# Optimization experiments

Measured on AMD Instinct MI355X. Metric: run time of the kernel, lower is better.

The kernel has to match this reference:

```python
import jax, jax.numpy as jnp
import numpy as np

N_NODES = 50000
N_EDGES = 800000
D = 128
N_LAYERS = 3
N_GRAPHS = 256


def setup_inputs() -> dict:
    key = jax.random.key(0)
    ks = jax.random.split(key, 6)
    x = jax.random.normal(ks[0], (N_NODES, D), dtype=jnp.float32)
    edge_index = jax.random.randint(ks[1], (2, N_EDGES), 0, N_NODES, dtype=jnp.int64)
    batch = jnp.sort(jax.random.randint(ks[2], (N_NODES,), 0, N_GRAPHS, dtype=jnp.int64))
    # Xavier-uniform linear weights (bias filled with 0 per weights_init)
    limit = float(np.sqrt(6.0 / (D + D)))
    W1 = jax.random.uniform(ks[3], (N_LAYERS, D, D), jnp.float32, -limit, limit)
    W2 = jax.random.uniform(ks[4], (N_LAYERS, D, D), jnp.float32, -limit, limit)
    b1 = jnp.zeros((N_LAYERS, D), jnp.float32)
    b2 = jnp.zeros((N_LAYERS, D), jnp.float32)
    return {"x": x, "edge_index": edge_index, "batch": batch,
            "W1": W1, "b1": b1, "W2": W2, "b2": b2}


def reference(x, edge_index, batch, W1, b1, W2, b2):
    src, dst = edge_index[0], edge_index[1]
    h = x  # [N, D]
    pools = []
    for i in range(N_LAYERS):
        # GINConv, eps=0: (1+eps)*h + sum of neighbor (source) features at target
        agg = jax.ops.segment_sum(h[src], dst, num_segments=N_NODES)  # [N, D]
        h = h + agg
        # MLP: Linear -> ReLU -> Linear, then outer ReLU activation
        h = jnp.maximum(h @ W1[i] + b1[i], 0.0) @ W2[i] + b2[i]
        h = jnp.maximum(h, 0.0)
        # global_add_pool over graph ids
        pools.append(jax.ops.segment_sum(h, batch, num_segments=N_GRAPHS))
    return jnp.concatenate(pools, axis=1)  # [N_GRAPHS, N_LAYERS*D]
```

## Files before the change

### kernel.cpp

```cpp
#include <hip/hip_runtime.h>

#define N_NODES 50000
#define N_EDGES 800000
#define DIM 128
#define N_LAYERS 3
#define N_GRAPHS 256
#define OUT_COLS (N_LAYERS * DIM)

#define SUBS 4
#define SUBCAP 24
#define ROWSTRIDE (SUBS * SUBCAP)

#define FILL_NB 3125
#define X2H_NB 6250
#define WPREP_NB 384

typedef __attribute__((ext_vector_type(8))) _Float16 half8;
typedef __attribute__((ext_vector_type(4))) float f32x4;
typedef __attribute__((ext_vector_type(4))) unsigned short us4;
typedef __attribute__((ext_vector_type(8))) short short8;

__global__ __launch_bounds__(256) void prep_kernel(
        const int* __restrict__ src, const int* __restrict__ dst,
        int* __restrict__ deg4, unsigned short* __restrict__ elist,
        const float* __restrict__ x, unsigned short* __restrict__ x16,
        const float* __restrict__ W1, const float* __restrict__ W2,
        _Float16* __restrict__ Wt) {
    const int b = blockIdx.x;
    if (b < FILL_NB) {
        int e = b * 256 + threadIdx.x;
        int d = dst[e];
        int s = src[e];
        int sub = e & (SUBS - 1);
        int r = atomicAdd(&deg4[d * SUBS + sub], 1);
        if (r < SUBCAP) elist[(size_t)d * ROWSTRIDE + sub * SUBCAP + r] = (unsigned short)s;
    } else if (b < FILL_NB + X2H_NB) {
        int i = (b - FILL_NB) * 256 + threadIdx.x;
        float4 v = *(const float4*)&x[(size_t)i * 4];
        us4 o;
        _Float16 h0 = (_Float16)v.x, h1 = (_Float16)v.y, h2 = (_Float16)v.z, h3 = (_Float16)v.w;
        o.x = *(unsigned short*)&h0; o.y = *(unsigned short*)&h1;
        o.z = *(unsigned short*)&h2; o.w = *(unsigned short*)&h3;
        *(us4*)&x16[(size_t)i * 4] = o;
    } else {
        int i = (b - FILL_NB - X2H_NB) * 256 + threadIdx.x;
        int which = i / (N_LAYERS * DIM * DIM);
        int rem = i % (N_LAYERS * DIM * DIM);
        int layer = rem / (DIM * DIM);
        int kj = rem % (DIM * DIM);
        int k = kj / DIM, j = kj % DIM;
        float w = (which ? W2 : W1)[rem];
        int lin = layer * 2 + which;
        Wt[(lin * DIM + j) * DIM + k] = (_Float16)w;
    }
}

__global__ __launch_bounds__(64, 3) void fused_layer_kernel(
        const unsigned short* __restrict__ hin, const int* __restrict__ deg4,
        const unsigned short* __restrict__ elist,
        const _Float16* __restrict__ Wt,
        const float* __restrict__ bias1, const float* __restrict__ bias2,
        const int* __restrict__ batch, unsigned short* __restrict__ h16out,
        float* __restrict__ pool_out, int layer, int write_h) {
    __shared__ float S[16][132];
    __shared__ int gb[16];
    const int l = threadIdx.x;
    const int lr = l & 15;
    const int lk = l >> 4;
    const int row0 = blockIdx.x * 16;

    if (l < 16) gb[l] = batch[row0 + l];

    const int node = row0 + lr;
    float acc[4][8];
    {
        const size_t sb = (size_t)node * DIM + lk * 8;
#pragma unroll
        for (int kb = 0; kb < 4; kb++) {
            half8 v = *(const half8*)&hin[sb + kb * 32];
#pragma unroll
            for (int j = 0; j < 8; j++) acc[kb][j] = (float)v[j];
        }
    }
    int4 c4 = *(const int4*)&deg4[node * SUBS];
    const unsigned short* elbase = &elist[(size_t)node * ROWSTRIDE];
#pragma unroll
    for (int sub = 0; sub < SUBS; sub++) {
        int cnt = ((const int*)&c4)[sub];
        if (cnt > SUBCAP) cnt = SUBCAP;
        const unsigned short* el = elbase + sub * SUBCAP;
        int i = 0;
        for (; i + 4 <= cnt; i += 4) {
            int s0 = el[i], s1 = el[i + 1], s2 = el[i + 2], s3 = el[i + 3];
            const size_t b0 = (size_t)s0 * DIM + lk * 8;
            const size_t b1 = (size_t)s1 * DIM + lk * 8;
            const size_t b2 = (size_t)s2 * DIM + lk * 8;
            const size_t b3 = (size_t)s3 * DIM + lk * 8;
            half8 v0[4], v1[4], v2[4], v3[4];
#pragma unroll
            for (int kb = 0; kb < 4; kb++) {
                v0[kb] = *(const half8*)&hin[b0 + kb * 32];
                v1[kb] = *(const half8*)&hin[b1 + kb * 32];
                v2[kb] = *(const half8*)&hin[b2 + kb * 32];
                v3[kb] = *(const half8*)&hin[b3 + kb * 32];
            }
#pragma unroll
            for (int kb = 0; kb < 4; kb++)
#pragma unroll
                for (int j = 0; j < 8; j++)
                    acc[kb][j] += ((float)v0[kb][j] + (float)v1[kb][j]) +
                                  ((float)v2[kb][j] + (float)v3[kb][j]);
        }
        for (; i < cnt; i++) {
            int s0 = el[i];
            const size_t b0 = (size_t)s0 * DIM + lk * 8;
#pragma unroll
            for (int kb = 0; kb < 4; kb++) {
                half8 v0 = *(const half8*)&hin[b0 + kb * 32];
#pragma unroll
                for (int j = 0; j < 8; j++) acc[kb][j] += (float)v0[j];
            }
        }
    }
    half8 ah[4];
#pragma unroll
    for (int kb = 0; kb < 4; kb++)
#pragma unroll
        for (int j = 0; j < 8; j++) ah[kb][j] = (_Float16)acc[kb][j];

#pragma unroll
    for (int cb = 0; cb < 8; cb++) {
        const _Float16* wp = &Wt[(cb * 16 + lr) * DIM + lk * 8];
        half8 w[4];
#pragma unroll
        for (int kb = 0; kb < 4; kb++) w[kb] = *(const half8*)&wp[kb * 32];
        f32x4 aA = {0.f, 0.f, 0.f, 0.f};
#pragma unroll
        for (int kb = 0; kb < 4; kb++)
            aA = __builtin_amdgcn_mfma_f32_16x16x32_f16(ah[kb], w[kb], aA, 0, 0, 0);
        float bv = bias1[cb * 16 + lr];
#pragma unroll
        for (int r = 0; r < 4; r++)
            S[lk * 4 + r][cb * 16 + lr] = fmaxf(aA[r] + bv, 0.f);
    }

    half8 ch[4], cl[4];
#pragma unroll
    for (int kb = 0; kb < 4; kb++) {
        const float* sr = &S[lr][kb * 32 + lk * 8];
        f32x4 u0 = *(const f32x4*)&sr[0];
        f32x4 u1 = *(const f32x4*)&sr[4];
        float uu[8] = {u0.x, u0.y, u0.z, u0.w, u1.x, u1.y, u1.z, u1.w};
        half8 hh, ll;
#pragma unroll
        for (int j = 0; j < 8; j++) {
            _Float16 hv = (_Float16)uu[j];
            hh[j] = hv;
            ll[j] = (_Float16)(uu[j] - (float)hv);
        }
        ch[kb] = hh;
        cl[kb] = ll;
    }

    const _Float16* W2 = Wt + DIM * DIM;
#pragma unroll
    for (int cb = 0; cb < 8; cb++) {
        const _Float16* wp = &W2[(cb * 16 + lr) * DIM + lk * 8];
        half8 w[4];
#pragma unroll
        for (int kb = 0; kb < 4; kb++) w[kb] = *(const half8*)&wp[kb * 32];
        f32x4 aA = {0.f, 0.f, 0.f, 0.f}, aC = aA;
#pragma unroll
        for (int kb = 0; kb < 4; kb++) {
            aA = __builtin_amdgcn_mfma_f32_16x16x32_f16(ch[kb], w[kb], aA, 0, 0, 0);
            aC = __builtin_amdgcn_mfma_f32_16x16x32_f16(cl[kb], w[kb], aC, 0, 0, 0);
        }
        float bv = bias2[cb * 16 + lr];
#pragma unroll
        for (int r = 0; r < 4; r++)
            S[lk * 4 + r][cb * 16 + lr] = fmaxf(aA[r] + aC[r] + bv, 0.f);
    }

    if (write_h) {
        const int r = l >> 2, c0 = (l & 3) * 32;
        unsigned short buf[32];
#pragma unroll
        for (int j = 0; j < 32; j++) {
            _Float16 hv = (_Float16)S[r][c0 + j];
            buf[j] = *(unsigned short*)&hv;
        }
        const size_t ob = (size_t)(row0 + r) * DIM + c0;
#pragma unroll
        for (int q = 0; q < 4; q++)
            *(short8*)&h16out[ob + q * 8] = *(const short8*)&buf[q * 8];
    }

    const int d0 = 2 * l;
    float p0 = 0.f, p1 = 0.f;
    int curg = gb[0];
    for (int r = 0; r < 16; r++) {
        int g = gb[r];
        if (g != curg) {
            atomicAdd(&pool_out[curg * OUT_COLS + layer * DIM + d0], p0);
            atomicAdd(&pool_out[curg * OUT_COLS + layer * DIM + d0 + 1], p1);
            p0 = p1 = 0.f;
            curg = g;
        }
        p0 += S[r][d0];
        p1 += S[r][d0 + 1];
    }
    atomicAdd(&pool_out[curg * OUT_COLS + layer * DIM + d0], p0);
    atomicAdd(&pool_out[curg * OUT_COLS + layer * DIM + d0 + 1], p1);
}


extern "C" void kernel_launch(void* const* d_in, const int* in_sizes, int n_in,
                              void* d_out, int out_size, void* d_ws, size_t ws_size,
                              hipStream_t stream) {
    const float* x = (const float*)d_in[0];
    const int* ei = (const int*)d_in[1];
    const int* batch = (const int*)d_in[2];
    const float* W1 = (const float*)d_in[3];
    const float* b1 = (const float*)d_in[4];
    const float* W2 = (const float*)d_in[5];
    const float* b2 = (const float*)d_in[6];
    float* out = (float*)d_out;

    const int* src = ei;
    const int* dst = ei + N_EDGES;

    char* ws = (char*)d_ws;
    unsigned short* x16 = (unsigned short*)ws;
    unsigned short* hA = (unsigned short*)(ws + 12800000);
    unsigned short* hB = (unsigned short*)(ws + 25600000);
    int* deg4 = (int*)(ws + 38400000);
    _Float16* Wt = (_Float16*)(ws + 39200000);
    unsigned short* elist = (unsigned short*)(ws + 39396608);

    hipMemsetAsync(d_out, 0, (size_t)out_size * sizeof(float), stream);
    hipMemsetAsync(deg4, 0, (size_t)N_NODES * SUBS * sizeof(int), stream);

    prep_kernel<<<FILL_NB + X2H_NB + WPREP_NB, 256, 0, stream>>>(
        src, dst, deg4, elist, x, x16, W1, W2, Wt);

    const int grid = N_NODES / 16;

    const unsigned short* hin[3] = {x16, hA, hB};
    unsigned short* hout[3] = {hA, hB, nullptr};
    for (int layer = 0; layer < N_LAYERS; layer++) {
        fused_layer_kernel<<<grid, 64, 0, stream>>>(
            hin[layer], deg4, elist, Wt + (size_t)layer * 2 * DIM * DIM,
            b1 + layer * DIM, b2 + layer * DIM, batch, hout[layer], out, layer,
            (layer < N_LAYERS - 1) ? 1 : 0);
    }
}
```

Baseline: 240.2 us.

## Split fused layer work across two wavefronts per 16-row block

Each block now runs two wavefronts instead of one. The feature dimension of the neighbor gather is split between them, and the partial aggregates are exchanged through shared memory. The output columns of both MLP GEMMs are split across the wavefronts as well. This halves per-thread register state and should raise occupancy and memory-level parallelism for the latency-bound gather. The cost is extra barriers and a shared-memory exchange buffer.

```diff
diff --git a/kernel.cpp b/kernel.cpp
--- a/kernel.cpp
+++ b/kernel.cpp
@@ -55,7 +55,7 @@
     }
 }
 
-__global__ __launch_bounds__(64, 3) void fused_layer_kernel(
+__global__ __launch_bounds__(128, 8) void fused_layer_kernel(
         const unsigned short* __restrict__ hin, const int* __restrict__ deg4,
         const unsigned short* __restrict__ elist,
         const _Float16* __restrict__ Wt,
@@ -63,23 +63,27 @@
         const int* __restrict__ batch, unsigned short* __restrict__ h16out,
         float* __restrict__ pool_out, int layer, int write_h) {
     __shared__ float S[16][132];
+    __shared__ _Float16 ex[4][64][8];
     __shared__ int gb[16];
-    const int l = threadIdx.x;
+    const int t = threadIdx.x;
+    const int w = t >> 6;
+    const int l = t & 63;
     const int lr = l & 15;
     const int lk = l >> 4;
     const int row0 = blockIdx.x * 16;
-
-    if (l < 16) gb[l] = batch[row0 + l];
+    const int kb0 = w * 2;
+
+    if (t < 16) gb[t] = batch[row0 + t];
 
     const int node = row0 + lr;
-    float acc[4][8];
+    float acc[2][8];
     {
-        const size_t sb = (size_t)node * DIM + lk * 8;
-#pragma unroll
-        for (int kb = 0; kb < 4; kb++) {
-            half8 v = *(const half8*)&hin[sb + kb * 32];
-#pragma unroll
-            for (int j = 0; j < 8; j++) acc[kb][j] = (float)v[j];
+        const size_t sb = (size_t)node * DIM + lk * 8 + kb0 * 32;
+#pragma unroll
+        for (int q = 0; q < 2; q++) {
+            half8 v = *(const half8*)&hin[sb + q * 32];
+#pragma unroll
+            for (int j = 0; j < 8; j++) acc[q][j] = (float)v[j];
         }
     }
     int4 c4 = *(const int4*)&deg4[node * SUBS];
@@ -92,57 +96,65 @@
         int i = 0;
         for (; i + 4 <= cnt; i += 4) {
             int s0 = el[i], s1 = el[i + 1], s2 = el[i + 2], s3 = el[i + 3];
-            const size_t b0 = (size_t)s0 * DIM + lk * 8;
-            const size_t b1 = (size_t)s1 * DIM + lk * 8;
-            const size_t b2 = (size_t)s2 * DIM + lk * 8;
-            const size_t b3 = (size_t)s3 * DIM + lk * 8;
-            half8 v0[4], v1[4], v2[4], v3[4];
-#pragma unroll
-            for (int kb = 0; kb < 4; kb++) {
-                v0[kb] = *(const half8*)&hin[b0 + kb * 32];
-                v1[kb] = *(const half8*)&hin[b1 + kb * 32];
-                v2[kb] = *(const half8*)&hin[b2 + kb * 32];
-                v3[kb] = *(const half8*)&hin[b3 + kb * 32];
+            const size_t b0 = (size_t)s0 * DIM + lk * 8 + kb0 * 32;
+            const size_t b1 = (size_t)s1 * DIM + lk * 8 + kb0 * 32;
+            const size_t b2 = (size_t)s2 * DIM + lk * 8 + kb0 * 32;
+            const size_t b3 = (size_t)s3 * DIM + lk * 8 + kb0 * 32;
+            half8 v0[2], v1[2], v2[2], v3[2];
+#pragma unroll
+            for (int q = 0; q < 2; q++) {
+                v0[q] = *(const half8*)&hin[b0 + q * 32];
+                v1[q] = *(const half8*)&hin[b1 + q * 32];
+                v2[q] = *(const half8*)&hin[b2 + q * 32];
+                v3[q] = *(const half8*)&hin[b3 + q * 32];
             }
 #pragma unroll
-            for (int kb = 0; kb < 4; kb++)
+            for (int q = 0; q < 2; q++)
 #pragma unroll
                 for (int j = 0; j < 8; j++)
-                    acc[kb][j] += ((float)v0[kb][j] + (float)v1[kb][j]) +
-                                  ((float)v2[kb][j] + (float)v3[kb][j]);
+                    acc[q][j] += ((float)v0[q][j] + (float)v1[q][j]) +
+                                 ((float)v2[q][j] + (float)v3[q][j]);
         }
         for (; i < cnt; i++) {
-            int s0 = el[i];
-            const size_t b0 = (size_t)s0 * DIM + lk * 8;
-#pragma unroll
-            for (int kb = 0; kb < 4; kb++) {
-                half8 v0 = *(const half8*)&hin[b0 + kb * 32];
-#pragma unroll
-                for (int j = 0; j < 8; j++) acc[kb][j] += (float)v0[j];
+            const size_t b0 = (size_t)el[i] * DIM + lk * 8 + kb0 * 32;
+#pragma unroll
+            for (int q = 0; q < 2; q++) {
+                half8 v0 = *(const half8*)&hin[b0 + q * 32];
+#pragma unroll
+                for (int j = 0; j < 8; j++) acc[q][j] += (float)v0[j];
             }
         }
     }
+#pragma unroll
+    for (int q = 0; q < 2; q++) {
+        half8 hv;
+#pragma unroll
+        for (int j = 0; j < 8; j++) hv[j] = (_Float16)acc[q][j];
+        *(half8*)&ex[kb0 + q][l][0] = hv;
+    }
+    __syncthreads();
+
     half8 ah[4];
 #pragma unroll
-    for (int kb = 0; kb < 4; kb++)
-#pragma unroll
-        for (int j = 0; j < 8; j++) ah[kb][j] = (_Float16)acc[kb][j];
-
-#pragma unroll
-    for (int cb = 0; cb < 8; cb++) {
+    for (int kb = 0; kb < 4; kb++) ah[kb] = *(const half8*)&ex[kb][l][0];
+
+#pragma unroll
+    for (int c = 0; c < 4; c++) {
+        const int cb = w * 4 + c;
         const _Float16* wp = &Wt[(cb * 16 + lr) * DIM + lk * 8];
-        half8 w[4];
-#pragma unroll
-        for (int kb = 0; kb < 4; kb++) w[kb] = *(const half8*)&wp[kb * 32];
+        half8 wv[4];
+#pragma unroll
+        for (int kb = 0; kb < 4; kb++) wv[kb] = *(const half8*)&wp[kb * 32];
         f32x4 aA = {0.f, 0.f, 0.f, 0.f};
 #pragma unroll
         for (int kb = 0; kb < 4; kb++)
-            aA = __builtin_amdgcn_mfma_f32_16x16x32_f16(ah[kb], w[kb], aA, 0, 0, 0);
+            aA = __builtin_amdgcn_mfma_f32_16x16x32_f16(ah[kb], wv[kb], aA, 0, 0, 0);
         float bv = bias1[cb * 16 + lr];
 #pragma unroll
         for (int r = 0; r < 4; r++)
             S[lk * 4 + r][cb * 16 + lr] = fmaxf(aA[r] + bv, 0.f);
     }
+    __syncthreads();
 
     half8 ch[4], cl[4];
 #pragma unroll
@@ -161,56 +173,55 @@
         ch[kb] = hh;
         cl[kb] = ll;
     }
+    __syncthreads();
 
     const _Float16* W2 = Wt + DIM * DIM;
 #pragma unroll
-    for (int cb = 0; cb < 8; cb++) {
+    for (int c = 0; c < 4; c++) {
+        const int cb = w * 4 + c;
         const _Float16* wp = &W2[(cb * 16 + lr) * DIM + lk * 8];
-        half8 w[4];
-#pragma unroll
-        for (int kb = 0; kb < 4; kb++) w[kb] = *(const half8*)&wp[kb * 32];
+        half8 wv[4];
+#pragma unroll
+        for (int kb = 0; kb < 4; kb++) wv[kb] = *(const half8*)&wp[kb * 32];
         f32x4 aA = {0.f, 0.f, 0.f, 0.f}, aC = aA;
 #pragma unroll
         for (int kb = 0; kb < 4; kb++) {
-            aA = __builtin_amdgcn_mfma_f32_16x16x32_f16(ch[kb], w[kb], aA, 0, 0, 0);
-            aC = __builtin_amdgcn_mfma_f32_16x16x32_f16(cl[kb], w[kb], aC, 0, 0, 0);
+            aA = __builtin_amdgcn_mfma_f32_16x16x32_f16(ch[kb], wv[kb], aA, 0, 0, 0);
+            aC = __builtin_amdgcn_mfma_f32_16x16x32_f16(cl[kb], wv[kb], aC, 0, 0, 0);
         }
         float bv = bias2[cb * 16 + lr];
 #pragma unroll
         for (int r = 0; r < 4; r++)
             S[lk * 4 + r][cb * 16 + lr] = fmaxf(aA[r] + aC[r] + bv, 0.f);
     }
+    __syncthreads();
 
     if (write_h) {
-        const int r = l >> 2, c0 = (l & 3) * 32;
-        unsigned short buf[32];
-#pragma unroll
-        for (int j = 0; j < 32; j++) {
+        const int r = t >> 3, c0 = (t & 7) * 16;
+        unsigned short buf[16];
+#pragma unroll
+        for (int j = 0; j < 16; j++) {
             _Float16 hv = (_Float16)S[r][c0 + j];
             buf[j] = *(unsigned short*)&hv;
         }
         const size_t ob = (size_t)(row0 + r) * DIM + c0;
-#pragma unroll
-        for (int q = 0; q < 4; q++)
-            *(short8*)&h16out[ob + q * 8] = *(const short8*)&buf[q * 8];
-    }
-
-    const int d0 = 2 * l;
-    float p0 = 0.f, p1 = 0.f;
+        *(short8*)&h16out[ob] = *(const short8*)&buf[0];
+        *(short8*)&h16out[ob + 8] = *(const short8*)&buf[8];
+    }
+
+    const int d0 = t;
+    float p0 = 0.f;
     int curg = gb[0];
     for (int r = 0; r < 16; r++) {
         int g = gb[r];
         if (g != curg) {
             atomicAdd(&pool_out[curg * OUT_COLS + layer * DIM + d0], p0);
-            atomicAdd(&pool_out[curg * OUT_COLS + layer * DIM + d0 + 1], p1);
-            p0 = p1 = 0.f;
+            p0 = 0.f;
             curg = g;
         }
         p0 += S[r][d0];
-        p1 += S[r][d0 + 1];
     }
     atomicAdd(&pool_out[curg * OUT_COLS + layer * DIM + d0], p0);
-    atomicAdd(&pool_out[curg * OUT_COLS + layer * DIM + d0 + 1], p1);
 }
 
 
@@ -248,7 +259,7 @@
     const unsigned short* hin[3] = {x16, hA, hB};
     unsigned short* hout[3] = {hA, hB, nullptr};
     for (int layer = 0; layer < N_LAYERS; layer++) {
-        fused_layer_kernel<<<grid, 64, 0, stream>>>(
+        fused_layer_kernel<<<grid, 128, 0, stream>>>(
             hin[layer], deg4, elist, Wt + (size_t)layer * 2 * DIM * DIM,
             b1 + layer * DIM, b2 + layer * DIM, batch, hout[layer], out, layer,
             (layer < N_LAYERS - 1) ? 1 : 0);
```

Result: slower. 259.0 us (+7.8%).
